# Kernel optimization log

Measured on AMD Instinct MI355X. Metric: run time of the kernel, lower is better.

Reference implementation:

```python
import jax, jax.numpy as jnp
import numpy as np

F, N, E = 8, 2048, 32768          # frames, atoms/frame, directed edges/frame
C, NT, NB, NSH = 32, 4, 8, 4      # channels, atom types, Bessel basis, (lmax+1)^2 for lmax=1
R_MAX, L_BOX, NUM_LAYERS = 6.0, 8.0, 3


def setup_inputs() -> dict:
    key = jax.random.key(0)
    ks = jax.random.split(key, 8)
    pos = jax.random.uniform(ks[0], (F, N, 3), jnp.float32) * L_BOX
    src = jax.random.randint(ks[1], (F, 1, E), 0, N)
    off = jax.random.randint(ks[2], (F, 1, E), 1, N)  # avoid self edges
    edge_index = jnp.concatenate([src, (src + off) % N], axis=1).astype(jnp.int32)
    cell = jnp.full((F, 3), L_BOX, jnp.float32)
    atom_types = jax.random.randint(ks[3], (F, N), 0, NT).astype(jnp.int32)
    W_embed = jax.random.normal(ks[4], (NT, C), jnp.float32) * 0.5
    W_rad = jax.random.normal(ks[5], (NUM_LAYERS, NB, C * NSH), jnp.float32) / np.sqrt(NB)
    W_mix = jax.random.normal(ks[6], (NUM_LAYERS, C, C), jnp.float32) / np.sqrt(C)
    w_out = jax.random.normal(ks[7], (C,), jnp.float32) / np.sqrt(C)
    return dict(pos=pos, edge_index=edge_index, cell=cell, atom_types=atom_types,
                W_embed=W_embed, W_rad=W_rad, W_mix=W_mix, w_out=w_out, cut_off=4)


def _atomic_energy(pos_flat, src, dst, shift, at_flat, W_embed, W_rad, W_mix, w_out):
    # edge vectors with (detached) PBC cell shift
    vec = pos_flat[dst] - pos_flat[src] + shift                      # [Et,3]
    r = jnp.sqrt(jnp.sum(vec * vec, -1) + 1e-12)                     # [Et]
    # spherical harmonics lmax=1, component normalization
    Y = jnp.concatenate([jnp.ones_like(r)[:, None],
                         np.sqrt(3.0) * vec / r[:, None]], axis=1)   # [Et,4]
    # Bessel radial basis with p=6 polynomial cutoff envelope
    x = r / R_MAX
    n = jnp.arange(1, NB + 1, dtype=pos_flat.dtype)
    bessel = np.sqrt(2.0 / R_MAX) * jnp.sin(n[None] * np.pi * x[:, None]) / r[:, None]
    env = (1.0 - 28.0 * x**6 + 48.0 * x**7 - 21.0 * x**8) * (x < 1.0).astype(pos_flat.dtype)
    basis = bessel * env[:, None]                                    # [Et,NB]
    FN = pos_flat.shape[0]
    h0 = jax.nn.one_hot(at_flat, NT, dtype=pos_flat.dtype) @ W_embed  # [FN,C]
    feat = jnp.zeros((FN, C, NSH), pos_flat.dtype).at[:, :, 0].set(h0)
    for l in range(NUM_LAYERS):
        R = (basis @ W_rad[l]).reshape(-1, C, NSH)                   # [Et,C,4]
        # gather scalar src feature, tensor-product with SH, radial weight
        msg = R * feat[src, :, 0][:, :, None] * Y[:, None, :]        # [Et,C,4]
        agg = jax.ops.segment_sum(msg, dst, num_segments=FN)         # scatter
        feat = feat + jnp.einsum('ncK,cd->ndK', agg, W_mix[l])       # resnet
    return feat[:, :, 0] @ w_out                                     # [FN]


def reference(pos, edge_index, cell, atom_types, W_embed, W_rad, W_mix, w_out, cut_off):
    Fn, Nn, Ee = pos.shape[0], pos.shape[1], edge_index.shape[2]
    pos_flat = pos.reshape(-1, 3)
    # offset edge indices per frame, flatten frame-major
    ei = (edge_index + (jnp.arange(Fn, dtype=edge_index.dtype) * Nn)[:, None, None])
    ei = ei.transpose(1, 0, 2).reshape(2, -1)
    src, dst = ei[0], ei[1]
    cell_e = jnp.repeat(cell, Ee, axis=0)                            # [F*E,3]
    co = jnp.asarray(cut_off, pos.dtype)
    v = pos_flat[dst] - pos_flat[src]
    shift = jax.lax.stop_gradient(
        cell_e * ((v < -co).astype(pos.dtype) - (v > co).astype(pos.dtype)))
    # symmetrize edges (both directions)
    src2 = jnp.concatenate([src, dst]); dst2 = jnp.concatenate([dst, src])
    shift2 = jnp.concatenate([shift, -shift], axis=0)
    at_flat = atom_types.reshape(-1)
    e_fn = lambda p: _atomic_energy(p, src2, dst2, shift2, at_flat,
                                    W_embed, W_rad, W_mix, w_out)
    atomic_e = e_fn(pos_flat)                                        # [F*N]
    total_energy = atomic_e.reshape(Fn, Nn).sum(axis=1)              # [F]
    force = -jax.grad(lambda p: e_fn(p).sum())(pos_flat)             # -dE/dpos
    return total_energy, force.reshape(Fn, Nn, 3)
```

## Files before the change

### kernel.cpp

```cpp
#include <hip/hip_runtime.h>
#include <math.h>

#define F_NUM 8
#define N_AT 2048
#define E_EDGE 32768
#define FE (F_NUM*E_EDGE)
#define FN (F_NUM*N_AT)
#define CAP 72
#define PI_F 3.14159265358979f

#if defined(__has_builtin)
#if __has_builtin(__builtin_amdgcn_fdot2)
#define HAS_FDOT2 1
#endif
#endif

typedef _Float16 h2 __attribute__((ext_vector_type(2)));

#define XSWZ(bid, G) (((bid) & 7) * ((G) >> 3) + ((bid) >> 3))

__device__ __forceinline__ unsigned short f2b(float x) {
    unsigned int u = __float_as_uint(x);
    u += 0x8000u;
    return (unsigned short)(u >> 16);
}
__device__ __forceinline__ float blo(unsigned int u) { return __uint_as_float(u << 16); }
__device__ __forceinline__ float bhi(unsigned int u) { return __uint_as_float(u & 0xffff0000u); }
__device__ __forceinline__ float b2f(unsigned short u) { return __uint_as_float((unsigned)u << 16); }

__device__ __forceinline__ unsigned f2h(float x) {
    union { _Float16 h; unsigned short u; } cv;
    cv.h = (_Float16)x;
    return (unsigned)cv.u;
}
__device__ __forceinline__ h2 u2h2(unsigned u) {
    union { unsigned u; h2 h; } cv;
    cv.u = u;
    return cv.h;
}
__device__ __forceinline__ float dot8h(uint4 q, const h2* w) {
#ifdef HAS_FDOT2
    float a = __builtin_amdgcn_fdot2(u2h2(q.x), w[0], 0.f, false);
    a = __builtin_amdgcn_fdot2(u2h2(q.y), w[1], a, false);
    a = __builtin_amdgcn_fdot2(u2h2(q.z), w[2], a, false);
    a = __builtin_amdgcn_fdot2(u2h2(q.w), w[3], a, false);
    return a;
#else
    h2 a0 = u2h2(q.x), a1 = u2h2(q.y), a2 = u2h2(q.z), a3 = u2h2(q.w);
    return (float)a0.x*(float)w[0].x + (float)a0.y*(float)w[0].y
         + (float)a1.x*(float)w[1].x + (float)a1.y*(float)w[1].y
         + (float)a2.x*(float)w[2].x + (float)a2.y*(float)w[2].y
         + (float)a3.x*(float)w[3].x + (float)a3.y*(float)w[3].y;
#endif
}
__device__ __forceinline__ void prep_wr(const float* __restrict__ Wrad_l, int c, h2* wr) {
#pragma unroll
    for (int bb = 0; bb < 4; bb++) {
        h2 t;
        t.x = (_Float16)Wrad_l[(2*bb)   * 128 + c * 4];
        t.y = (_Float16)Wrad_l[(2*bb+1) * 128 + c * 4];
        wr[bb] = t;
    }
}

__global__ __launch_bounds__(256) void k_zg(
    int4* __restrict__ cnt4, const float* __restrict__ w_out,
    const float* __restrict__ Wmix2, float* __restrict__ g2)
{
    int bid = blockIdx.x;
    if (bid < 16) {
        cnt4[bid * 256 + threadIdx.x] = make_int4(0, 0, 0, 0);
    } else if (threadIdx.x < 32) {
        int c = threadIdx.x;
        float acc = 0.f;
#pragma unroll
        for (int d = 0; d < 32; d++) acc += w_out[d] * Wmix2[c * 32 + d];
        g2[c] = acc;
    }
}


__global__ __launch_bounds__(256) void k_edges(
    const float* __restrict__ pos, const int* __restrict__ eidx,
    const float* __restrict__ cell, const int* __restrict__ co_p,
    const int* __restrict__ at,
    uint4* __restrict__ dbq, float4* __restrict__ unit, uint2* __restrict__ ab,
    int* __restrict__ cnt, uint4* __restrict__ rec)
{
    int bid = XSWZ(blockIdx.x, FE / 256);
    int k = bid * 256 + threadIdx.x;
    int f = k >> 15;
    int e = k & (E_EDGE - 1);
    int a = eidx[f * 2 * E_EDGE + e] + f * N_AT;
    int b = eidx[f * 2 * E_EDGE + E_EDGE + e] + f * N_AT;
    int ta = at[a], tb = at[b];
    float co = (float)co_p[0];

    float vec[3];
#pragma unroll
    for (int d = 0; d < 3; d++) {
        float v  = pos[3 * b + d] - pos[3 * a + d];
        float cl = cell[3 * f + d];
        float sh = cl * ((v < -co ? 1.f : 0.f) - (v > co ? 1.f : 0.f));
        vec[d] = v + sh;
    }
    float r2   = vec[0]*vec[0] + vec[1]*vec[1] + vec[2]*vec[2] + 1e-12f;
    float r    = sqrtf(r2);
    float rinv = 1.f / r;
    unit[k] = make_float4(vec[0]*rinv, vec[1]*rinv, vec[2]*rinv, 0.f);
    ab[k] = make_uint2((unsigned)((a << 2) | ta), (unsigned)((b << 2) | tb));

    float x = r * (1.f / 6.f);
    float env = 0.f, denv = 0.f;
    if (x < 1.f) {
        float x2 = x*x, x3 = x2*x, x5 = x2*x3, x6 = x5*x, x7 = x6*x, x8 = x7*x;
        env  = 1.f - 28.f*x6 + 48.f*x7 - 21.f*x8;
        denv = -168.f*x5 + 336.f*x6 - 168.f*x7;
    }
    float s1, c1;
    sincosf(PI_F * x, &s1, &c1);
    float sn = s1, cn = c1;
    const float C0 = 0.57735026919f;
    float bs[8], db[8];
#pragma unroll
    for (int n = 1; n <= 8; n++) {
        float kn  = (float)n * PI_F * (1.f / 6.f);
        float bes = C0 * sn * rinv;
        bs[n-1] = bes * env;
        db[n-1] = C0 * rinv * (kn * cn - sn * rinv) * env + bes * denv * (1.f / 6.f);
        float sn2 = sn * c1 + cn * s1;
        float cn2 = cn * c1 - sn * s1;
        sn = sn2; cn = cn2;
    }
    uint4 B, D;
    B.x = f2h(bs[0]) | (f2h(bs[1]) << 16);
    B.y = f2h(bs[2]) | (f2h(bs[3]) << 16);
    B.z = f2h(bs[4]) | (f2h(bs[5]) << 16);
    B.w = f2h(bs[6]) | (f2h(bs[7]) << 16);
    D.x = f2h(db[0]) | (f2h(db[1]) << 16);
    D.y = f2h(db[2]) | (f2h(db[3]) << 16);
    D.z = f2h(db[4]) | (f2h(db[5]) << 16);
    D.w = f2h(db[6]) | (f2h(db[7]) << 16);
    dbq[k] = D;

    int sa = atomicAdd(&cnt[a], 1);
    if (sa < CAP) {
        int ia = 2 * (a * CAP + sa);
        rec[ia]     = make_uint4((unsigned)((b << 3) | tb), B.x, B.y, B.z);
        rec[ia + 1] = make_uint4(B.w, (unsigned)(k << 1), 0, 0);
    }
    int sb = atomicAdd(&cnt[b], 1);
    if (sb < CAP) {
        int ib = 2 * (b * CAP + sb);
        rec[ib]     = make_uint4((unsigned)((a << 3) | 4 | ta), B.x, B.y, B.z);
        rec[ib + 1] = make_uint4(B.w, (unsigned)((k << 1) | 1), 0, 0);
    }
}

#define LOADREC(J, NB, B)                                    \
    {                                                        \
        uint4 ra = rec[2*(J)], rb = rec[2*(J)+1];            \
        NB = (int)ra.x;                                      \
        B  = make_uint4(ra.y, ra.z, ra.w, rb.x);             \
    }

__global__ __launch_bounds__(512) void k_L0(
    const float* __restrict__ W_embed, unsigned short* __restrict__ soq,
    const int* __restrict__ cnt, const uint4* __restrict__ rec,
    const float* __restrict__ Wrad_l, const float* __restrict__ Wmix_l,
    const int* __restrict__ at)
{
    __shared__ float We[128];
    int t = threadIdx.x;
    if (t < 128) We[t] = W_embed[t];
    int bid = XSWZ(blockIdx.x, FN / 64);
    int g = t >> 5, c = t & 31;
    int abase = bid * 64;
    h2 wr[4];
    prep_wr(Wrad_l, c, wr);
    float wv[32];
#pragma unroll
    for (int cc = 0; cc < 32; ++cc) wv[cc] = Wmix_l[cc * 32 + c];
    __syncthreads();

    for (int i = 0; i < 4; ++i) {
        int n = abase + g * 4 + i;
        int cn = min(cnt[n], CAP);
        int j = n * CAP, j1 = n * CAP + cn;
        float A = 0.f;
        for (; j + 3 < j1; j += 4) {
            int n0, n1, n2, n3;
            uint4 b0, b1, b2, b3;
            LOADREC(j, n0, b0) LOADREC(j+1, n1, b1) LOADREC(j+2, n2, b2) LOADREC(j+3, n3, b3)
            A += dot8h(b0, wr) * We[(n0 & 3) * 32 + c] + dot8h(b1, wr) * We[(n1 & 3) * 32 + c]
               + dot8h(b2, wr) * We[(n2 & 3) * 32 + c] + dot8h(b3, wr) * We[(n3 & 3) * 32 + c];
        }
        for (; j < j1; ++j) {
            int n0; uint4 b0;
            LOADREC(j, n0, b0)
            A += dot8h(b0, wr) * We[(n0 & 3) * 32 + c];
        }
        float acc = 0.f;
#pragma unroll
        for (int cc = 0; cc < 32; ++cc) acc += __shfl(A, cc, 32) * wv[cc];
        soq[n * 32 + c] = f2b(We[at[n] * 32 + c] + acc);
    }
}


__global__ __launch_bounds__(512) void k_L1s(
    const unsigned short* __restrict__ slq, unsigned short* __restrict__ soq,
    const int* __restrict__ cnt, const uint4* __restrict__ rec,
    const float* __restrict__ Wrad_l, const float* __restrict__ Wmix_l)
{
    extern __shared__ unsigned short feat[];
    int t = threadIdx.x;
    int bid = XSWZ(blockIdx.x, 256);
    int frame = bid >> 5;
    int fat = frame * N_AT;
    int abase = fat + (bid & 31) * 64;
    const uint4* src = (const uint4*)(slq + (size_t)fat * 32);
    uint4* dst = (uint4*)feat;
#pragma unroll
    for (int it = 0; it < 16; ++it) dst[t + it * 512] = src[t + it * 512];
    int g = t >> 5, c = t & 31;
    h2 wr[4];
    prep_wr(Wrad_l, c, wr);
    float wv[32];
#pragma unroll
    for (int cc = 0; cc < 32; ++cc) wv[cc] = Wmix_l[cc * 32 + c];
    __syncthreads();

    for (int i = 0; i < 4; ++i) {
        int n = abase + g * 4 + i;
        int cn = min(cnt[n], CAP);
        int j = n * CAP, j1 = n * CAP + cn;
        float A = 0.f;
        for (; j + 3 < j1; j += 4) {
            int n0, n1, n2, n3;
            uint4 b0, b1, b2, b3;
            LOADREC(j, n0, b0) LOADREC(j+1, n1, b1) LOADREC(j+2, n2, b2) LOADREC(j+3, n3, b3)
            float sv0 = b2f(feat[((n0 >> 3) - fat) * 32 + c]);
            float sv1 = b2f(feat[((n1 >> 3) - fat) * 32 + c]);
            float sv2 = b2f(feat[((n2 >> 3) - fat) * 32 + c]);
            float sv3 = b2f(feat[((n3 >> 3) - fat) * 32 + c]);
            A += dot8h(b0, wr) * sv0 + dot8h(b1, wr) * sv1
               + dot8h(b2, wr) * sv2 + dot8h(b3, wr) * sv3;
        }
        for (; j < j1; ++j) {
            int n0; uint4 b0;
            LOADREC(j, n0, b0)
            A += dot8h(b0, wr) * b2f(feat[((n0 >> 3) - fat) * 32 + c]);
        }
        float acc = 0.f;
#pragma unroll
        for (int cc = 0; cc < 32; ++cc) acc += __shfl(A, cc, 32) * wv[cc];
        float base_s = b2f(feat[(n - fat) * 32 + c]);
        soq[n * 32 + c] = f2b(base_s + acc);
    }
}

__global__ __launch_bounds__(512) void k_L2Es(
    const unsigned short* __restrict__ s2q,
    const int* __restrict__ cnt, const uint4* __restrict__ rec,
    const float* __restrict__ Wrad2, const float* __restrict__ Wmix1,
    const float* __restrict__ w_out, const float* __restrict__ g2,
    float* __restrict__ barS2, unsigned short* __restrict__ ba1q, float* __restrict__ epart)
{
    extern __shared__ unsigned short feat[];
    int t = threadIdx.x;
    int bid = XSWZ(blockIdx.x, 256);
    int frame = bid >> 5;
    int fat = frame * N_AT;
    int abase = fat + (bid & 31) * 64;
    const uint4* src = (const uint4*)(s2q + (size_t)fat * 32);
    uint4* dst = (uint4*)feat;
#pragma unroll
    for (int it = 0; it < 16; ++it) dst[t + it * 512] = src[t + it * 512];
    int g = t >> 5, c = t & 31;
    h2 wr[4];
    prep_wr(Wrad2, c, wr);
    float wv[32];
#pragma unroll
    for (int d = 0; d < 32; ++d) wv[d] = Wmix1[c * 32 + d];
    float woc = w_out[c], g2c = g2[c];
    __syncthreads();

    for (int i = 0; i < 4; ++i) {
        int n = abase + g * 4 + i;
        int cn = min(cnt[n], CAP);
        int j = n * CAP, j1 = n * CAP + cn;
        float A = 0.f, S = 0.f;
        for (; j + 3 < j1; j += 4) {
            int n0, n1, n2, n3;
            uint4 b0, b1, b2, b3;
            LOADREC(j, n0, b0) LOADREC(j+1, n1, b1) LOADREC(j+2, n2, b2) LOADREC(j+3, n3, b3)
            float r0 = dot8h(b0, wr), r1 = dot8h(b1, wr), r2 = dot8h(b2, wr), r3 = dot8h(b3, wr);
            A += r0 * b2f(feat[((n0 >> 3) - fat) * 32 + c]) + r1 * b2f(feat[((n1 >> 3) - fat) * 32 + c])
               + r2 * b2f(feat[((n2 >> 3) - fat) * 32 + c]) + r3 * b2f(feat[((n3 >> 3) - fat) * 32 + c]);
            S += r0 + r1 + r2 + r3;
        }
        for (; j < j1; ++j) {
            int n0; uint4 b0;
            LOADREC(j, n0, b0)
            float rr = dot8h(b0, wr);
            A += rr * b2f(feat[((n0 >> 3) - fat) * 32 + c]);
            S += rr;
        }
        float s2n = b2f(feat[(n - fat) * 32 + c]);
        float te = s2n * woc + A * g2c;
#pragma unroll
        for (int o = 1; o <= 16; o <<= 1) te += __shfl_xor(te, o, 32);
        if (c == 0) epart[n] = te;
        float bs2 = woc + g2c * S;
        barS2[n * 32 + c] = bs2;
        float acc = 0.f;
#pragma unroll
        for (int d = 0; d < 32; ++d) acc += __shfl(bs2, d, 32) * wv[d];
        ba1q[n * 32 + c] = f2b(acc);
    }
}

__global__ __launch_bounds__(512) void k_B1Fs(
    const unsigned short* __restrict__ ba1q, const float* __restrict__ barS2,
    const unsigned short* __restrict__ s1q, const unsigned short* __restrict__ s2q,
    const int* __restrict__ cnt, const uint4* __restrict__ rec,
    const float* __restrict__ Wrad1, const float* __restrict__ Wmix0,
    uint2* __restrict__ pk)
{
    extern __shared__ unsigned short feat[];
    int t = threadIdx.x;
    int bid = XSWZ(blockIdx.x, 256);
    int frame = bid >> 5;
    int fat = frame * N_AT;
    int abase = fat + (bid & 31) * 64;
    const uint4* src = (const uint4*)(ba1q + (size_t)fat * 32);
    uint4* dst = (uint4*)feat;
#pragma unroll
    for (int it = 0; it < 16; ++it) dst[t + it * 512] = src[t + it * 512];
    int g = t >> 5, c = t & 31;
    h2 wr[4];
    prep_wr(Wrad1, c, wr);
    float wv[32];
#pragma unroll
    for (int d = 0; d < 32; ++d) wv[d] = Wmix0[c * 32 + d];
    __syncthreads();

    for (int i = 0; i < 4; ++i) {
        int n = abase + g * 4 + i;
        int cn = min(cnt[n], CAP);
        int j = n * CAP, j1 = n * CAP + cn;
        float A = 0.f;
        for (; j + 3 < j1; j += 4) {
            int n0, n1, n2, n3;
            uint4 b0, b1, b2, b3;
            LOADREC(j, n0, b0) LOADREC(j+1, n1, b1) LOADREC(j+2, n2, b2) LOADREC(j+3, n3, b3)
            A += dot8h(b0, wr) * b2f(feat[((n0 >> 3) - fat) * 32 + c])
               + dot8h(b1, wr) * b2f(feat[((n1 >> 3) - fat) * 32 + c])
               + dot8h(b2, wr) * b2f(feat[((n2 >> 3) - fat) * 32 + c])
               + dot8h(b3, wr) * b2f(feat[((n3 >> 3) - fat) * 32 + c]);
        }
        for (; j < j1; ++j) {
            int n0; uint4 b0;
            LOADREC(j, n0, b0)
            A += dot8h(b0, wr) * b2f(feat[((n0 >> 3) - fat) * 32 + c]);
        }
        int n32c = n * 32 + c;
        float bs1 = barS2[n32c] + A;
        float acc = 0.f;
#pragma unroll
        for (int d = 0; d < 32; ++d) acc += __shfl(bs1, d, 32) * wv[d];
        uint2 v;
        v.x = (unsigned)s1q[n32c] | ((unsigned)s2q[n32c] << 16);
        v.y = (unsigned)f2b(acc)  | ((unsigned)feat[(n - fat) * 32 + c] << 16);
        pk[n32c] = v;
    }
}

#define EPG 8
__global__ __launch_bounds__(256, 4) void k_force_e(
    const uint2* __restrict__ pk, const float* __restrict__ g2,
    const uint4* __restrict__ dbq, const uint2* __restrict__ ab,
    const float4* __restrict__ unit,
    const float* __restrict__ W_embed, const float* __restrict__ W_rad,
    float4* __restrict__ fvec)
{
    __shared__ float We[128];
    int t = threadIdx.x;
    if (t < 128) We[t] = W_embed[t];
    int bid = XSWZ(blockIdx.x, FE / (8 * EPG));
    int g = t >> 5;
    int c = t & 31;
    h2 wr0[4], wr1[4], wr2[4];
    prep_wr(W_rad + 0 * 1024, c, wr0);
    prep_wr(W_rad + 1 * 1024, c, wr1);
    prep_wr(W_rad + 2 * 1024, c, wr2);
    float g2c = g2[c];
    __syncthreads();

    int kbase = (bid * 8 + g) * EPG;
    uint2 e2a[EPG];
#pragma unroll
    for (int kk = 0; kk < EPG; ++kk) e2a[kk] = ab[kbase + kk];
    uint2 qa[EPG], qb[EPG];
    uint4 dd[EPG];
#pragma unroll
    for (int kk = 0; kk < EPG; ++kk) {
        qa[kk] = pk[(e2a[kk].x >> 2) * 32 + c];
        qb[kk] = pk[(e2a[kk].y >> 2) * 32 + c];
        dd[kk] = dbq[kbase + kk];
    }
#pragma unroll
    for (int kk = 0; kk < EPG; ++kk) {
        int k = kbase + kk;
        uint2 e2 = e2a[kk];
        float s0a = We[(e2.x & 3) * 32 + c];
        float s0b = We[(e2.y & 3) * 32 + c];
        float dR0 = dot8h(dd[kk], wr0), dR1 = dot8h(dd[kk], wr1), dR2 = dot8h(dd[kk], wr2);
        float tc = dR0 * (blo(qa[kk].y) * s0b + blo(qb[kk].y) * s0a)
                 + dR1 * (bhi(qa[kk].y) * blo(qb[kk].x) + bhi(qb[kk].y) * blo(qa[kk].x))
                 + dR2 * g2c * (bhi(qa[kk].x) + bhi(qb[kk].x));
#pragma unroll
        for (int o = 1; o <= 16; o <<= 1) tc += __shfl_xor(tc, o, 32);
        if (c < 4) {
            float uval = ((const float*)unit)[4 * k + c];
            ((float*)fvec)[4 * k + c] = tc * uval;
        }
    }
}

__global__ __launch_bounds__(256, 8) void k_fgat(
    const int* __restrict__ cnt, const uint4* __restrict__ rec,
    const float4* __restrict__ fvec,
    const float* __restrict__ epart, float* __restrict__ out)
{
    if (blockIdx.x >= FN / 8) {
        __shared__ float sm[256];
        int f = blockIdx.x - FN / 8, t = threadIdx.x;
        float a = 0.f;
        for (int i = t; i < N_AT; i += 256) a += epart[f * N_AT + i];
        sm[t] = a;
        __syncthreads();
        for (int s = 128; s; s >>= 1) {
            if (t < s) sm[t] += sm[t + s];
            __syncthreads();
        }
        if (t == 0) out[f] = sm[0];
        return;
    }
    int t = threadIdx.x;
    int bid = XSWZ(blockIdx.x, FN / 8);
    int g = t >> 5, lane = t & 31;
    int n = bid * 8 + g;
    int cn = min(cnt[n], CAP);
    int base = n * CAP;
    float Fx = 0.f, Fy = 0.f, Fz = 0.f;
    for (int j = base + lane; j < base + cn; j += 32) {
        unsigned s = rec[2 * j + 1].y;
        int k = (int)(s >> 1);
        float sg = (s & 1) ? -1.f : 1.f;
        float4 fv = fvec[k];
        Fx += sg * fv.x; Fy += sg * fv.y; Fz += sg * fv.z;
    }
#pragma unroll
    for (int o = 1; o <= 16; o <<= 1) {
        Fx += __shfl_xor(Fx, o, 32);
        Fy += __shfl_xor(Fy, o, 32);
        Fz += __shfl_xor(Fz, o, 32);
    }
    if (lane == 0) {
        out[8 + n * 3 + 0] = Fx;
        out[8 + n * 3 + 1] = Fy;
        out[8 + n * 3 + 2] = Fz;
    }
}

extern "C" void kernel_launch(void* const* d_in, const int* in_sizes, int n_in,
                              void* d_out, int out_size, void* d_ws, size_t ws_size,
                              hipStream_t stream)
{
    const float* pos     = (const float*)d_in[0];
    const int*   eidx    = (const int*)  d_in[1];
    const float* cell    = (const float*)d_in[2];
    const int*   at      = (const int*)  d_in[3];
    const float* W_embed = (const float*)d_in[4];
    const float* W_rad   = (const float*)d_in[5];
    const float* W_mix   = (const float*)d_in[6];
    const float* w_out   = (const float*)d_in[7];
    const int*   co      = (const int*)  d_in[8];

    char* p = (char*)d_ws;
    auto carve = [&](size_t bytes) -> char* {
        char* r = p;
        p += (bytes + 255) & ~(size_t)255;
        return r;
    };
    uint4*          dbq    = (uint4*)          carve((size_t)FE * 16);
    float4*         unit   = (float4*)         carve((size_t)FE * 16);
    float4*         fvec   = (float4*)         carve((size_t)FE * 16);
    uint2*          ab     = (uint2*)          carve((size_t)FE * 8);
    unsigned short* s1q    = (unsigned short*) carve((size_t)FN * 32 * 2);
    unsigned short* s2q    = (unsigned short*) carve((size_t)FN * 32 * 2);
    unsigned short* ba1q   = (unsigned short*) carve((size_t)FN * 32 * 2);
    float*          barS2  = (float*)          carve((size_t)FN * 32 * 4);
    uint2*          pk     = (uint2*)          carve((size_t)FN * 32 * 8);
    float*          g2     = (float*)          carve(32 * 4);
    float*          epart  = (float*)          carve((size_t)FN * 4);
    int*            cnt    = (int*)            carve((size_t)FN * 4);
    uint4*          rec    = (uint4*)          carve((size_t)FN * CAP * 32);

    const size_t SMEM = (size_t)N_AT * 32 * 2;

    k_zg<<<17, 256, 0, stream>>>((int4*)cnt, w_out, W_mix + 2 * 1024, g2);

    k_edges<<<FE / 256, 256, 0, stream>>>(pos, eidx, cell, co, at, dbq, unit, ab, cnt, rec);

    k_L0<<<FN / 64, 512, 0, stream>>>(W_embed, s1q, cnt, rec,
                                      W_rad + 0 * 1024, W_mix + 0 * 1024, at);
    k_L1s<<<256, 512, SMEM, stream>>>(s1q, s2q, cnt, rec,
                                      W_rad + 1 * 1024, W_mix + 1 * 1024);
    k_L2Es<<<256, 512, SMEM, stream>>>(s2q, cnt, rec, W_rad + 2 * 1024,
                                       W_mix + 1 * 1024, w_out, g2, barS2, ba1q, epart);
    k_B1Fs<<<256, 512, SMEM, stream>>>(ba1q, barS2, s1q, s2q, cnt, rec,
                                       W_rad + 1 * 1024, W_mix + 0 * 1024, pk);
    k_force_e<<<FE / (8 * EPG), 256, 0, stream>>>(pk, g2, dbq, ab, unit, W_embed, W_rad, fvec);
    k_fgat<<<FN / 8 + F_NUM, 256, 0, stream>>>(cnt, rec, fvec, epart, (float*)d_out);
}
```

Before: 179.3 us.

## Scatter edge force scalars into per-atom slots and store fp16 unit vectors in records

```diff
diff --git a/kernel.cpp b/kernel.cpp
--- a/kernel.cpp
+++ b/kernel.cpp
@@ -84,7 +84,7 @@
     const float* __restrict__ pos, const int* __restrict__ eidx,
     const float* __restrict__ cell, const int* __restrict__ co_p,
     const int* __restrict__ at,
-    uint4* __restrict__ dbq, float4* __restrict__ unit, uint2* __restrict__ ab,
+    uint4* __restrict__ dbq, uint2* __restrict__ ab, uint2* __restrict__ jsl,
     int* __restrict__ cnt, uint4* __restrict__ rec)
 {
     int bid = XSWZ(blockIdx.x, FE / 256);
@@ -107,7 +107,11 @@
     float r2   = vec[0]*vec[0] + vec[1]*vec[1] + vec[2]*vec[2] + 1e-12f;
     float r    = sqrtf(r2);
     float rinv = 1.f / r;
-    unit[k] = make_float4(vec[0]*rinv, vec[1]*rinv, vec[2]*rinv, 0.f);
+    float ux = vec[0]*rinv, uy = vec[1]*rinv, uz = vec[2]*rinv;
+    unsigned up01 = f2h(ux)  | (f2h(uy)  << 16);
+    unsigned up2  = f2h(uz);
+    unsigned un01 = f2h(-ux) | (f2h(-uy) << 16);
+    unsigned un2  = f2h(-uz);
     ab[k] = make_uint2((unsigned)((a << 2) | ta), (unsigned)((b << 2) | tb));
 
     float x = r * (1.f / 6.f);
@@ -144,17 +148,22 @@
     dbq[k] = D;
 
     int sa = atomicAdd(&cnt[a], 1);
+    unsigned ja = (unsigned)(FN * CAP);
     if (sa < CAP) {
-        int ia = 2 * (a * CAP + sa);
-        rec[ia]     = make_uint4((unsigned)((b << 3) | tb), B.x, B.y, B.z);
-        rec[ia + 1] = make_uint4(B.w, (unsigned)(k << 1), 0, 0);
+        int j = a * CAP + sa;
+        ja = (unsigned)j;
+        rec[2*j]     = make_uint4((unsigned)((b << 3) | tb), B.x, B.y, B.z);
+        rec[2*j + 1] = make_uint4(B.w, up01, up2, 0);
     }
     int sb = atomicAdd(&cnt[b], 1);
+    unsigned jb = (unsigned)(FN * CAP);
     if (sb < CAP) {
-        int ib = 2 * (b * CAP + sb);
-        rec[ib]     = make_uint4((unsigned)((a << 3) | 4 | ta), B.x, B.y, B.z);
-        rec[ib + 1] = make_uint4(B.w, (unsigned)((k << 1) | 1), 0, 0);
-    }
+        int j = b * CAP + sb;
+        jb = (unsigned)j;
+        rec[2*j]     = make_uint4((unsigned)((a << 3) | 4 | ta), B.x, B.y, B.z);
+        rec[2*j + 1] = make_uint4(B.w, un01, un2, 0);
+    }
+    jsl[k] = make_uint2(ja, jb);
 }
 
 #define LOADREC(J, NB, B)                                    \
@@ -377,13 +386,13 @@
     }
 }
 
-#define EPG 8
-__global__ __launch_bounds__(256, 4) void k_force_e(
+#define EPG 4
+__global__ __launch_bounds__(256, 8) void k_force_e(
     const uint2* __restrict__ pk, const float* __restrict__ g2,
     const uint4* __restrict__ dbq, const uint2* __restrict__ ab,
-    const float4* __restrict__ unit,
+    const uint2* __restrict__ jsl,
     const float* __restrict__ W_embed, const float* __restrict__ W_rad,
-    float4* __restrict__ fvec)
+    float* __restrict__ hEdr)
 {
     __shared__ float We[128];
     int t = threadIdx.x;
@@ -399,39 +408,31 @@
     __syncthreads();
 
     int kbase = (bid * 8 + g) * EPG;
-    uint2 e2a[EPG];
-#pragma unroll
-    for (int kk = 0; kk < EPG; ++kk) e2a[kk] = ab[kbase + kk];
-    uint2 qa[EPG], qb[EPG];
-    uint4 dd[EPG];
-#pragma unroll
-    for (int kk = 0; kk < EPG; ++kk) {
-        qa[kk] = pk[(e2a[kk].x >> 2) * 32 + c];
-        qb[kk] = pk[(e2a[kk].y >> 2) * 32 + c];
-        dd[kk] = dbq[kbase + kk];
-    }
 #pragma unroll
     for (int kk = 0; kk < EPG; ++kk) {
         int k = kbase + kk;
-        uint2 e2 = e2a[kk];
+        uint2 e2 = ab[k];
+        int a = (int)(e2.x >> 2), b = (int)(e2.y >> 2);
+        uint4 d  = dbq[k];
+        uint2 qa = pk[a * 32 + c];
+        uint2 qb = pk[b * 32 + c];
         float s0a = We[(e2.x & 3) * 32 + c];
         float s0b = We[(e2.y & 3) * 32 + c];
-        float dR0 = dot8h(dd[kk], wr0), dR1 = dot8h(dd[kk], wr1), dR2 = dot8h(dd[kk], wr2);
-        float tc = dR0 * (blo(qa[kk].y) * s0b + blo(qb[kk].y) * s0a)
-                 + dR1 * (bhi(qa[kk].y) * blo(qb[kk].x) + bhi(qb[kk].y) * blo(qa[kk].x))
-                 + dR2 * g2c * (bhi(qa[kk].x) + bhi(qb[kk].x));
+        float dR0 = dot8h(d, wr0), dR1 = dot8h(d, wr1), dR2 = dot8h(d, wr2);
+        float tc = dR0 * (blo(qa.y) * s0b + blo(qb.y) * s0a)
+                 + dR1 * (bhi(qa.y) * blo(qb.x) + bhi(qb.y) * blo(qa.x))
+                 + dR2 * g2c * (bhi(qa.x) + bhi(qb.x));
 #pragma unroll
         for (int o = 1; o <= 16; o <<= 1) tc += __shfl_xor(tc, o, 32);
-        if (c < 4) {
-            float uval = ((const float*)unit)[4 * k + c];
-            ((float*)fvec)[4 * k + c] = tc * uval;
-        }
+        uint2 jv = jsl[k];
+        if (c == 0) hEdr[jv.x] = tc;
+        else if (c == 1) hEdr[jv.y] = tc;
     }
 }
 
 __global__ __launch_bounds__(256, 8) void k_fgat(
     const int* __restrict__ cnt, const uint4* __restrict__ rec,
-    const float4* __restrict__ fvec,
+    const float* __restrict__ hEdr,
     const float* __restrict__ epart, float* __restrict__ out)
 {
     if (blockIdx.x >= FN / 8) {
@@ -456,11 +457,12 @@
     int base = n * CAP;
     float Fx = 0.f, Fy = 0.f, Fz = 0.f;
     for (int j = base + lane; j < base + cn; j += 32) {
-        unsigned s = rec[2 * j + 1].y;
-        int k = (int)(s >> 1);
-        float sg = (s & 1) ? -1.f : 1.f;
-        float4 fv = fvec[k];
-        Fx += sg * fv.x; Fy += sg * fv.y; Fz += sg * fv.z;
+        uint4 r1 = rec[2 * j + 1];
+        float d = hEdr[j];
+        h2 uxy = u2h2(r1.y);
+        Fx += d * (float)uxy.x;
+        Fy += d * (float)uxy.y;
+        Fz += d * (float)u2h2(r1.z).x;
     }
 #pragma unroll
     for (int o = 1; o <= 16; o <<= 1) {
@@ -496,9 +498,8 @@
         return r;
     };
     uint4*          dbq    = (uint4*)          carve((size_t)FE * 16);
-    float4*         unit   = (float4*)         carve((size_t)FE * 16);
-    float4*         fvec   = (float4*)         carve((size_t)FE * 16);
     uint2*          ab     = (uint2*)          carve((size_t)FE * 8);
+    uint2*          jsl    = (uint2*)          carve((size_t)FE * 8);
     unsigned short* s1q    = (unsigned short*) carve((size_t)FN * 32 * 2);
     unsigned short* s2q    = (unsigned short*) carve((size_t)FN * 32 * 2);
     unsigned short* ba1q   = (unsigned short*) carve((size_t)FN * 32 * 2);
@@ -506,6 +507,7 @@
     uint2*          pk     = (uint2*)          carve((size_t)FN * 32 * 8);
     float*          g2     = (float*)          carve(32 * 4);
     float*          epart  = (float*)          carve((size_t)FN * 4);
+    float*          hEdr   = (float*)          carve((size_t)(FN * CAP + 8) * 4);
     int*            cnt    = (int*)            carve((size_t)FN * 4);
     uint4*          rec    = (uint4*)          carve((size_t)FN * CAP * 32);
 
@@ -513,7 +515,7 @@
 
     k_zg<<<17, 256, 0, stream>>>((int4*)cnt, w_out, W_mix + 2 * 1024, g2);
 
-    k_edges<<<FE / 256, 256, 0, stream>>>(pos, eidx, cell, co, at, dbq, unit, ab, cnt, rec);
+    k_edges<<<FE / 256, 256, 0, stream>>>(pos, eidx, cell, co, at, dbq, ab, jsl, cnt, rec);
 
     k_L0<<<FN / 64, 512, 0, stream>>>(W_embed, s1q, cnt, rec,
                                       W_rad + 0 * 1024, W_mix + 0 * 1024, at);
@@ -523,6 +525,6 @@
                                        W_mix + 1 * 1024, w_out, g2, barS2, ba1q, epart);
     k_B1Fs<<<256, 512, SMEM, stream>>>(ba1q, barS2, s1q, s2q, cnt, rec,
                                        W_rad + 1 * 1024, W_mix + 0 * 1024, pk);
-    k_force_e<<<FE / (8 * EPG), 256, 0, stream>>>(pk, g2, dbq, ab, unit, W_embed, W_rad, fvec);
-    k_fgat<<<FN / 8 + F_NUM, 256, 0, stream>>>(cnt, rec, fvec, epart, (float*)d_out);
-}
+    k_force_e<<<FE / (8 * EPG), 256, 0, stream>>>(pk, g2, dbq, ab, jsl, W_embed, W_rad, hEdr);
+    k_fgat<<<FN / 8 + F_NUM, 256, 0, stream>>>(cnt, rec, hEdr, epart, (float*)d_out);
+}
```

New measurement: 196.3 us. 9.5% more time.
